# Optimization experiments

Hardware: AMD Instinct MI355X
Metric: run time of the kernel (lower is better)

The kernel has to match this reference:

```python
import jax, jax.numpy as jnp
import numpy as np

B, C, H, W = 8, 128, 192, 192
CROP = 39
LEN = CROP // 2            # 19 -> 38x38 crop
CY = CX = 96               # fixed crop center (original draws random.randint(19, 173))
MARGIN = 1.0


def grid_sample_bilinear(img, grid):
    """Bilinear grid_sample, align_corners=True, zeros padding.
    img: (B,C,H,W); grid: (B,H,W,2) with (x,y) in [-1,1]."""
    _, _, Hi, Wi = img.shape
    gx = (grid[..., 0] + 1.0) * 0.5 * (Wi - 1)   # (B,H,W) source x
    gy = (grid[..., 1] + 1.0) * 0.5 * (Hi - 1)   # (B,H,W) source y
    x0 = jnp.floor(gx)
    y0 = jnp.floor(gy)

    def gather(xf, yf):
        valid = (xf >= 0) & (xf <= Wi - 1) & (yf >= 0) & (yf <= Hi - 1)
        xi = jnp.clip(xf, 0, Wi - 1).astype(jnp.int32)
        yi = jnp.clip(yf, 0, Hi - 1).astype(jnp.int32)
        # per-batch gather: (C,H,W) values at integer (y,x) locations
        v = jax.vmap(lambda im, y, x: im[:, y, x])(img, yi, xi)  # (B,C,H,W)
        return v * valid[:, None, :, :].astype(img.dtype)

    wx1 = gx - x0
    wx0 = 1.0 - wx1
    wy1 = gy - y0
    wy0 = 1.0 - wy1
    w = lambda a: a[:, None, :, :]
    return (w(wx0 * wy0) * gather(x0,       y0)
          + w(wx1 * wy0) * gather(x0 + 1.0, y0)
          + w(wx0 * wy1) * gather(x0,       y0 + 1.0)
          + w(wx1 * wy1) * gather(x0 + 1.0, y0 + 1.0))


def hardnet_loss(anchor, positive, margin=MARGIN):
    """loss_HardNet with anchor_swap=False, batch_reduce='min', triplet_margin."""
    d1 = jnp.sum(anchor * anchor, axis=1)                       # (N,)
    d2 = jnp.sum(positive * positive, axis=1)                   # (N,)
    sq = d1[:, None] + d2[None, :] - 2.0 * (anchor @ positive.T)  # (N,N)
    dm = jnp.sqrt(jnp.maximum(sq, 0.0) + 1e-6) + 1e-8
    n = dm.shape[0]
    pos = jnp.diagonal(dm)                                      # positive distances
    dmod = dm + jnp.eye(n, dtype=dm.dtype) * 10.0               # mask diagonal
    dmod = dmod + jnp.where(dmod < 0.008, 10.0, 0.0)            # mask near-duplicates
    min_neg = jnp.min(dmod, axis=1)                             # hardest negative per anchor
    return jnp.mean(jnp.maximum(margin + pos - min_neg, 0.0))


def setup_inputs() -> dict:
    key = jax.random.key(0)
    k1, k2, k3 = jax.random.split(key, 3)
    feat1 = jax.random.normal(k1, (B, C, H, W), dtype=jnp.float32)
    feat2 = jax.random.normal(k2, (B, C, H, W), dtype=jnp.float32)
    # absolute flow: pixel coordinates in [0, W-1] / [0, H-1]
    aflow = jax.random.uniform(k3, (B, 2, H, W), dtype=jnp.float32) * (W - 1)
    return {"feat1": feat1, "feat2": feat2, "aflow": aflow}


def reference(feat1, feat2, aflow):
    # _aflow_to_grid: pixel coords -> [-1,1] grid (align_corners=True convention)
    gx = aflow[:, 0] * (2.0 / (W - 1)) - 1.0
    gy = aflow[:, 1] * (2.0 / (H - 1)) - 1.0
    grid = jnp.stack([gx, gy], axis=-1)                          # (B,H,W,2)
    grid = jnp.where(jnp.isnan(grid), 9e9, grid)                 # invalid -> out of range
    feat2to1 = grid_sample_bilinear(feat2, grid)                 # warp img2 feats to img1
    s = slice(CY - LEN, CY + LEN)                                # fixed 38x38 crop
    f1 = feat1[:, :, s, s]
    f2 = feat2to1[:, :, s, s]
    a = f1.transpose(0, 2, 3, 1).reshape(-1, C)                  # (B*38*38, C)
    p = f2.transpose(0, 2, 3, 1).reshape(-1, C)
    return hardnet_loss(a, p)
```

## Files before the change

### kernel.cpp

```cpp
#include <hip/hip_runtime.h>
#include <stdint.h>

#define Hh 192
#define Ww 192
#define HW 36864
#define CROPW 38
#define CW2 1444
#define CROPOFF 77
#define NPTS 11552
#define NPAD 11776
#define NTT 46
#define NCT 92
#define NG 5
#define JPB 19
#define NBLK (NG*NTT)
#define CROPB 304
#define CRDB 46
#define BIGF 3.0e38f

typedef short bf16x8 __attribute__((ext_vector_type(8)));
typedef float f32x4 __attribute__((ext_vector_type(4)));
typedef uint32_t u32x2 __attribute__((ext_vector_type(2)));
typedef uint32_t u32x4 __attribute__((ext_vector_type(4)));
typedef unsigned short ushort;

__device__ __forceinline__ ushort f2bf(float f) {
  uint32_t b = __float_as_uint(f);
  uint32_t r = b + 0x7fffu + ((b >> 16) & 1u);
  return (ushort)(r >> 16);
}
__device__ __forceinline__ float bf2f(ushort u) {
  return __uint_as_float(((uint32_t)u) << 16);
}

__device__ __forceinline__ void g2l16(const void* g, void* l) {
  __builtin_amdgcn_global_load_lds(
      (const __attribute__((address_space(1))) unsigned int*)g,
      (__attribute__((address_space(3))) unsigned int*)l, 16, 0, 0);
}

__global__ __launch_bounds__(256) void prep2_k(
    const float* __restrict__ feat1, const float* __restrict__ aflow,
    ushort* __restrict__ aB, u32x4* __restrict__ coords) {
  int bid = blockIdx.x;
  int t = threadIdx.x;
  if (bid < CROPB) {
    __shared__ __align__(16) ushort lsh[38*136];
    int b = bid / CROPW, r = bid % CROPW;
    int y = CROPOFF + r;
    {
      int xo = t & 63, c0 = t >> 6;
      if (xo < CROPW) {
        const float* src = feat1 + ((size_t)b*128*HW) + (size_t)y*Ww + CROPOFF + xo;
        #pragma unroll
        for (int k = 0; k < 32; ++k) {
          int cc = c0*32 + k;
          lsh[xo*136 + cc] = f2bf(src[(size_t)cc*HW]);
        }
      }
    }
    __syncthreads();
    int chunk = t & 7, p0 = t >> 3;
    #pragma unroll
    for (int pp = 0; pp < 2; ++pp) {
      int p = p0 + pp*32;
      if (p >= CROPW) break;
      int idx = b*CW2 + r*CROPW + p;
      ushort* dst = aB + (size_t)idx*128 + chunk*16;
      *(bf16x8*)dst       = *(const bf16x8*)&lsh[p*136 + chunk*16];
      *(bf16x8*)(dst + 8) = *(const bf16x8*)&lsh[p*136 + chunk*16 + 8];
    }
  } else {
    int idx = (bid - CROPB)*256 + t;
    if (idx >= NPTS) return;
    int b = idx / CW2;
    int rem = idx % CW2;
    int r = rem / CROPW, cx = rem % CROPW;
    int y = CROPOFF + r, x = CROPOFF + cx;
    float ax = aflow[((b*2 + 0)*Hh + y)*Ww + x];
    float ay = aflow[((b*2 + 1)*Hh + y)*Ww + x];
    float gxn = ax * (2.0f/(Ww-1)) - 1.0f;
    float gyn = ay * (2.0f/(Hh-1)) - 1.0f;
    float gx = (gxn + 1.0f) * 0.5f * (Ww-1);
    float gy = (gyn + 1.0f) * 0.5f * (Hh-1);
    int xi = min((int)floorf(gx), Ww-2);
    int yi = min((int)floorf(gy), Hh-2);
    u32x4 cd;
    cd.x = (uint32_t)(yi*Ww + xi);
    cd.y = __float_as_uint(gx - (float)xi);
    cd.z = __float_as_uint(gy - (float)yi);
    cd.w = 0;
    coords[idx] = cd;
  }
}

__global__ __launch_bounds__(256) void slab_k(
    const float* __restrict__ feat2, const u32x4* __restrict__ coords,
    ushort* __restrict__ pB) {
  __shared__ __align__(16) ushort plane[HW];
  int bid = blockIdx.x;
  int b = bid >> 7, c = bid & 127;
  int t = threadIdx.x;
  const float* src = feat2 + ((size_t)(b*128 + c)) * HW;
  #pragma unroll
  for (int k = 0; k < 36; ++k) {
    int i = (k*256 + t) * 4;
    f32x4 v = *(const f32x4*)(src + i);
    u32x2 pk;
    pk.x = (uint32_t)f2bf(v[0]) | ((uint32_t)f2bf(v[1]) << 16);
    pk.y = (uint32_t)f2bf(v[2]) | ((uint32_t)f2bf(v[3]) << 16);
    *(u32x2*)&plane[i] = pk;
  }
  __syncthreads();
  int pbase = b*CW2;
  #pragma unroll
  for (int it = 0; it < 6; ++it) {
    int p = it*256 + t;
    if (p < CW2) {
      u32x4 cd = coords[pbase + p];
      int cell = (int)cd.x;
      float wx1 = __uint_as_float(cd.y), wx0 = 1.f - wx1;
      float wy1 = __uint_as_float(cd.z), wy0 = 1.f - wy1;
      float v00 = bf2f(plane[cell]);
      float v01 = bf2f(plane[cell + 1]);
      float v10 = bf2f(plane[cell + Ww]);
      float v11 = bf2f(plane[cell + Ww + 1]);
      float v = wy0*(wx0*v00 + wx1*v01) + wy1*(wx0*v10 + wx1*v11);
      pB[(size_t)(pbase + p)*128 + c] = f2bf(v);
    }
  }
}

__global__ __launch_bounds__(256) void d12_k(
    ushort* __restrict__ aB, ushort* __restrict__ pB,
    float* __restrict__ d1, float* __restrict__ d2) {
  int w = threadIdx.x >> 6, l = threadIdx.x & 63;
  int base = blockIdx.x*32 + w*8;
  #pragma unroll
  for (int i = 0; i < 8; ++i) {
    int row = base + i;
    if (row < NPTS) {
      uint32_t ua = *(const uint32_t*)&aB[(size_t)row*128 + l*2];
      uint32_t up = *(const uint32_t*)&pB[(size_t)row*128 + l*2];
      float a0 = bf2f((ushort)ua), a1 = bf2f((ushort)(ua >> 16));
      float p0 = bf2f((ushort)up), p1 = bf2f((ushort)(up >> 16));
      float sa = a0*a0 + a1*a1;
      float sp = p0*p0 + p1*p1;
      for (int off = 1; off < 64; off <<= 1) {
        sa += __shfl_xor(sa, off);
        sp += __shfl_xor(sp, off);
      }
      if (l == 0) { d1[row] = sa; d2[row] = sp; }
    } else {
      *(uint32_t*)&aB[(size_t)row*128 + l*2] = 0;
      *(uint32_t*)&pB[(size_t)row*128 + l*2] = 0;
      if (l == 0) { d1[row] = 0.f; d2[row] = 1e30f; }
    }
  }
}

__global__ __launch_bounds__(512) void gemmp_k(
    const ushort* __restrict__ aB, const ushort* __restrict__ pB,
    const float* __restrict__ d1, const float* __restrict__ d2,
    float* __restrict__ pos, float* __restrict__ pmin) {
  __shared__ __align__(16) ushort lB[2][128*128];

  int bid = blockIdx.x;
  int xcd = bid & 7, kk = bid >> 3;
  int start = (xcd < 6) ? xcd*29 : 174 + (xcd-6)*28;
  int L = start + kk;
  int g = L / NTT, tM = L % NTT;
  int j0 = g * JPB;
  int jn = (NCT - j0 < JPB) ? (NCT - j0) : JPB;

  int tid = threadIdx.x;
  int rowg = tid >> 4, cb = (tid & 15) << 4;
  int w = tid >> 6, l = tid & 63;
  int wr = w >> 1, wc = w & 1;
  int lcol = l & 15, hq = l >> 4, rb = hq << 2;
  int rsw = (lcol & 7) << 4;

  {
    const char* gB = (const char*)pB + (size_t)j0 * 128 * 256;
    #pragma unroll
    for (int rnd = 0; rnd < 4; ++rnd) {
      int row = rnd*32 + rowg;
      g2l16(gB + row*256 + (cb ^ ((row&7)<<4)), (char*)lB[0] + row*256 + cb);
    }
  }

  bf16x8 aF[16];
  {
    const char* gA = (const char*)aB + ((size_t)(tM*256 + wr*64 + lcol))*256 + hq*16;
    #pragma unroll
    for (int ma = 0; ma < 4; ++ma)
      #pragma unroll
      for (int ks = 0; ks < 4; ++ks)
        aF[ma*4+ks] = *(const bf16x8*)(gA + ma*16*256 + ks*64);
  }
  __syncthreads();

  float mPart[4] = {BIGF, BIGF, BIGF, BIGF};

  for (int it = 0; it < jn; ++it) {
    int j = j0 + it;
    if (it + 1 < jn) {
      const char* gB = (const char*)pB + (size_t)(j+1) * 128 * 256;
      char* dst = (char*)lB[(it+1) & 1];
      #pragma unroll
      for (int rnd = 0; rnd < 4; ++rnd) {
        int row = rnd*32 + rowg;
        g2l16(gB + row*256 + (cb ^ ((row&7)<<4)), dst + row*256 + cb);
      }
    }
    const char* bufB = (const char*)lB[it & 1];
    f32x4 acc[4][4] = {};
    #pragma unroll
    for (int ks = 0; ks < 4; ++ks) {
      int cbase = ks*64 + (hq << 4);
      bf16x8 bF[4];
      #pragma unroll
      for (int np = 0; np < 4; ++np)
        bF[np] = *(const bf16x8*)(bufB + (wc*64 + np*16 + lcol)*256 + (cbase ^ rsw));
      #pragma unroll
      for (int np = 0; np < 4; ++np)
        #pragma unroll
        for (int ma = 0; ma < 4; ++ma)
          acc[np][ma] = __builtin_amdgcn_mfma_f32_16x16x32_bf16(bF[np], aF[ma*4+ks], acc[np][ma], 0, 0, 0);
    }

    f32x4 d2v[4];
    #pragma unroll
    for (int np = 0; np < 4; ++np)
      d2v[np] = *(const f32x4*)&d2[j*128 + wc*64 + np*16 + rb];

    if ((j >> 1) != tM) {
      #pragma unroll
      for (int ma = 0; ma < 4; ++ma)
        #pragma unroll
        for (int np = 0; np < 4; ++np)
          #pragma unroll
          for (int reg = 0; reg < 4; ++reg)
            mPart[ma] = fminf(mPart[ma], fmaf(-2.f, acc[np][ma][reg], d2v[np][reg]));
    } else {
      #pragma unroll
      for (int ma = 0; ma < 4; ++ma) {
        int gi = tM*256 + wr*64 + ma*16 + lcol;
        #pragma unroll
        for (int np = 0; np < 4; ++np)
          #pragma unroll
          for (int reg = 0; reg < 4; ++reg) {
            int gj = j*128 + wc*64 + np*16 + rb + reg;
            float t = fmaf(-2.f, acc[np][ma][reg], d2v[np][reg]);
            if (gi == gj)
              pos[gi] = sqrtf(fmaxf(d1[gi] + t, 0.f) + 1e-6f) + 1e-8f;
            else
              mPart[ma] = fminf(mPart[ma], t);
          }
      }
    }
    __syncthreads();
  }

  #pragma unroll
  for (int ma = 0; ma < 4; ++ma) {
    float u = mPart[ma];
    u = fminf(u, __shfl_xor(u, 16));
    u = fminf(u, __shfl_xor(u, 32));
    mPart[ma] = u;
  }
  __syncthreads();
  float* sm = (float*)lB;
  if (hq == 0) {
    #pragma unroll
    for (int ma = 0; ma < 4; ++ma)
      sm[wc*256 + wr*64 + ma*16 + lcol] = mPart[ma];
  }
  __syncthreads();
  if (tid < 256) {
    int row = tM*256 + tid;
    float u = fminf(sm[tid], sm[256 + tid]);
    pmin[g*NPAD + row] = sqrtf(fmaxf(d1[row] + u, 0.f) + 1e-6f) + 1e-8f;
  }
}

__global__ __launch_bounds__(1024) void fin_k(const float* __restrict__ pos,
                                              const float* __restrict__ pmin,
                                              float* __restrict__ out) {
  float s = 0.f;
  for (int i = threadIdx.x; i < NPTS; i += 1024) {
    float p = pos[i];
    float mneg = p + 10.f;
    #pragma unroll
    for (int g = 0; g < NG; ++g) mneg = fminf(mneg, pmin[g*NPAD + i]);
    s += fmaxf(1.0f + p - mneg, 0.f);
  }
  for (int off = 1; off < 64; off <<= 1) s += __shfl_xor(s, off);
  __shared__ float red[16];
  if ((threadIdx.x & 63) == 0) red[threadIdx.x >> 6] = s;
  __syncthreads();
  if (threadIdx.x == 0) {
    float t = 0.f;
    #pragma unroll
    for (int k = 0; k < 16; ++k) t += red[k];
    out[0] = t / (float)NPTS;
  }
}

extern "C" void kernel_launch(void* const* d_in, const int* in_sizes, int n_in,
                              void* d_out, int out_size, void* d_ws, size_t ws_size,
                              hipStream_t stream) {
  const float* feat1 = (const float*)d_in[0];
  const float* feat2 = (const float*)d_in[1];
  const float* aflow = (const float*)d_in[2];

  char* ws = (char*)d_ws;
  ushort* aB = (ushort*)ws;
  ushort* pB = aB + (size_t)NPAD * 128;
  float*  d1 = (float*)(pB + (size_t)NPAD * 128);
  float*  d2 = d1 + NPAD;
  float*  pos = d2 + NPAD;
  float*  pmin = pos + NPAD;
  u32x4*  coords = (u32x4*)(pmin + (size_t)NG*NPAD);

  hipLaunchKernelGGL(prep2_k, dim3(CROPB + CRDB), dim3(256), 0, stream,
                     feat1, aflow, aB, coords);
  hipLaunchKernelGGL(slab_k, dim3(1024), dim3(256), 0, stream,
                     feat2, coords, pB);
  hipLaunchKernelGGL(d12_k, dim3(NPAD/32), dim3(256), 0, stream,
                     aB, pB, d1, d2);
  hipLaunchKernelGGL(gemmp_k, dim3(NBLK), dim3(512), 0, stream,
                     aB, pB, d1, d2, pos, pmin);
  hipLaunchKernelGGL(fin_k, dim3(1), dim3(1024), 0, stream,
                     pos, pmin, (float*)d_out);
}
```

Before: 98.19 us.

## Fuse norm computation into prep and warp kernels, pair channels, shrink GEMM tiles

```diff
diff --git a/kernel.cpp b/kernel.cpp
--- a/kernel.cpp
+++ b/kernel.cpp
@@ -9,11 +9,11 @@
 #define CROPOFF 77
 #define NPTS 11552
 #define NPAD 11776
-#define NTT 46
+#define NMT 92
 #define NCT 92
 #define NG 5
 #define JPB 19
-#define NBLK (NG*NTT)
+#define NBLK (NG*NMT)
 #define CROPB 304
 #define CRDB 46
 #define BIGF 3.0e38f
@@ -41,7 +41,9 @@
 
 __global__ __launch_bounds__(256) void prep2_k(
     const float* __restrict__ feat1, const float* __restrict__ aflow,
-    ushort* __restrict__ aB, u32x4* __restrict__ coords) {
+    ushort* __restrict__ aB, ushort* __restrict__ pB,
+    float* __restrict__ d1, float* __restrict__ d2,
+    u32x4* __restrict__ coords) {
   int bid = blockIdx.x;
   int t = threadIdx.x;
   if (bid < CROPB) {
@@ -69,10 +71,19 @@
       ushort* dst = aB + (size_t)idx*128 + chunk*16;
       *(bf16x8*)dst       = *(const bf16x8*)&lsh[p*136 + chunk*16];
       *(bf16x8*)(dst + 8) = *(const bf16x8*)&lsh[p*136 + chunk*16 + 8];
-    }
-  } else {
+      float s = 0.f;
+      #pragma unroll
+      for (int j = 0; j < 16; ++j) {
+        float v = bf2f(lsh[p*136 + chunk*16 + j]);
+        s += v*v;
+      }
+      s += __shfl_xor(s, 1); s += __shfl_xor(s, 2); s += __shfl_xor(s, 4);
+      if (chunk == 0) d1[idx] = s;
+    }
+  } else if (bid < CROPB + CRDB) {
     int idx = (bid - CROPB)*256 + t;
     if (idx >= NPTS) return;
+    d2[idx] = 0.f;
     int b = idx / CW2;
     int rem = idx % CW2;
     int r = rem / CROPW, cx = rem % CROPW;
@@ -91,25 +102,42 @@
     cd.z = __float_as_uint(gy - (float)yi);
     cd.w = 0;
     coords[idx] = cd;
+  } else {
+    if (t < NPAD - NPTS) {
+      int row = NPTS + t;
+      u32x4 z = {0,0,0,0};
+      #pragma unroll
+      for (int c = 0; c < 8; ++c) {
+        *(u32x4*)&aB[(size_t)row*128 + c*16] = z;
+        *(u32x4*)&aB[(size_t)row*128 + c*16 + 8] = z;
+        *(u32x4*)&pB[(size_t)row*128 + c*16] = z;
+        *(u32x4*)&pB[(size_t)row*128 + c*16 + 8] = z;
+      }
+      d1[row] = 0.f;
+      d2[row] = 1e30f;
+    }
   }
 }
 
 __global__ __launch_bounds__(256) void slab_k(
     const float* __restrict__ feat2, const u32x4* __restrict__ coords,
-    ushort* __restrict__ pB) {
-  __shared__ __align__(16) ushort plane[HW];
+    ushort* __restrict__ pB, float* __restrict__ d2) {
+  __shared__ __align__(16) uint32_t plane[HW];
   int bid = blockIdx.x;
-  int b = bid >> 7, c = bid & 127;
+  int b = bid >> 6, cp = bid & 63, c = cp*2;
   int t = threadIdx.x;
-  const float* src = feat2 + ((size_t)(b*128 + c)) * HW;
-  #pragma unroll
+  const float* srcA = feat2 + ((size_t)(b*128 + c)) * HW;
+  const float* srcB = srcA + HW;
+  #pragma unroll 6
   for (int k = 0; k < 36; ++k) {
     int i = (k*256 + t) * 4;
-    f32x4 v = *(const f32x4*)(src + i);
-    u32x2 pk;
-    pk.x = (uint32_t)f2bf(v[0]) | ((uint32_t)f2bf(v[1]) << 16);
-    pk.y = (uint32_t)f2bf(v[2]) | ((uint32_t)f2bf(v[3]) << 16);
-    *(u32x2*)&plane[i] = pk;
+    f32x4 va = *(const f32x4*)(srcA + i);
+    f32x4 vb = *(const f32x4*)(srcB + i);
+    u32x4 pk;
+    #pragma unroll
+    for (int j = 0; j < 4; ++j)
+      pk[j] = (uint32_t)f2bf(va[j]) | ((uint32_t)f2bf(vb[j]) << 16);
+    *(u32x4*)&plane[i] = pk;
   }
   __syncthreads();
   int pbase = b*CW2;
@@ -121,45 +149,23 @@
       int cell = (int)cd.x;
       float wx1 = __uint_as_float(cd.y), wx0 = 1.f - wx1;
       float wy1 = __uint_as_float(cd.z), wy0 = 1.f - wy1;
-      float v00 = bf2f(plane[cell]);
-      float v01 = bf2f(plane[cell + 1]);
-      float v10 = bf2f(plane[cell + Ww]);
-      float v11 = bf2f(plane[cell + Ww + 1]);
-      float v = wy0*(wx0*v00 + wx1*v01) + wy1*(wx0*v10 + wx1*v11);
-      pB[(size_t)(pbase + p)*128 + c] = f2bf(v);
-    }
-  }
-}
-
-__global__ __launch_bounds__(256) void d12_k(
-    ushort* __restrict__ aB, ushort* __restrict__ pB,
-    float* __restrict__ d1, float* __restrict__ d2) {
-  int w = threadIdx.x >> 6, l = threadIdx.x & 63;
-  int base = blockIdx.x*32 + w*8;
-  #pragma unroll
-  for (int i = 0; i < 8; ++i) {
-    int row = base + i;
-    if (row < NPTS) {
-      uint32_t ua = *(const uint32_t*)&aB[(size_t)row*128 + l*2];
-      uint32_t up = *(const uint32_t*)&pB[(size_t)row*128 + l*2];
-      float a0 = bf2f((ushort)ua), a1 = bf2f((ushort)(ua >> 16));
-      float p0 = bf2f((ushort)up), p1 = bf2f((ushort)(up >> 16));
-      float sa = a0*a0 + a1*a1;
-      float sp = p0*p0 + p1*p1;
-      for (int off = 1; off < 64; off <<= 1) {
-        sa += __shfl_xor(sa, off);
-        sp += __shfl_xor(sp, off);
-      }
-      if (l == 0) { d1[row] = sa; d2[row] = sp; }
-    } else {
-      *(uint32_t*)&aB[(size_t)row*128 + l*2] = 0;
-      *(uint32_t*)&pB[(size_t)row*128 + l*2] = 0;
-      if (l == 0) { d1[row] = 0.f; d2[row] = 1e30f; }
-    }
-  }
-}
-
-__global__ __launch_bounds__(512) void gemmp_k(
+      uint32_t u00 = plane[cell];
+      uint32_t u01 = plane[cell + 1];
+      uint32_t u10 = plane[cell + Ww];
+      uint32_t u11 = plane[cell + Ww + 1];
+      float v0 = wy0*(wx0*bf2f((ushort)u00) + wx1*bf2f((ushort)u01))
+               + wy1*(wx0*bf2f((ushort)u10) + wx1*bf2f((ushort)u11));
+      float v1 = wy0*(wx0*bf2f((ushort)(u00>>16)) + wx1*bf2f((ushort)(u01>>16)))
+               + wy1*(wx0*bf2f((ushort)(u10>>16)) + wx1*bf2f((ushort)(u11>>16)));
+      ushort q0 = f2bf(v0), q1 = f2bf(v1);
+      *(uint32_t*)&pB[(size_t)(pbase + p)*128 + c] = (uint32_t)q0 | ((uint32_t)q1 << 16);
+      float f0 = bf2f(q0), f1 = bf2f(q1);
+      atomicAdd(&d2[pbase + p], f0*f0 + f1*f1);
+    }
+  }
+}
+
+__global__ __launch_bounds__(256) void gemmp_k(
     const ushort* __restrict__ aB, const ushort* __restrict__ pB,
     const float* __restrict__ d1, const float* __restrict__ d2,
     float* __restrict__ pos, float* __restrict__ pmin) {
@@ -167,9 +173,9 @@
 
   int bid = blockIdx.x;
   int xcd = bid & 7, kk = bid >> 3;
-  int start = (xcd < 6) ? xcd*29 : 174 + (xcd-6)*28;
+  int start = (xcd < 4) ? xcd*58 : 232 + (xcd-4)*57;
   int L = start + kk;
-  int g = L / NTT, tM = L % NTT;
+  int g = L / NMT, tM = L % NMT;
   int j0 = g * JPB;
   int jn = (NCT - j0 < JPB) ? (NCT - j0) : JPB;
 
@@ -183,15 +189,15 @@
   {
     const char* gB = (const char*)pB + (size_t)j0 * 128 * 256;
     #pragma unroll
-    for (int rnd = 0; rnd < 4; ++rnd) {
-      int row = rnd*32 + rowg;
+    for (int rnd = 0; rnd < 8; ++rnd) {
+      int row = rnd*16 + rowg;
       g2l16(gB + row*256 + (cb ^ ((row&7)<<4)), (char*)lB[0] + row*256 + cb);
     }
   }
 
   bf16x8 aF[16];
   {
-    const char* gA = (const char*)aB + ((size_t)(tM*256 + wr*64 + lcol))*256 + hq*16;
+    const char* gA = (const char*)aB + ((size_t)(tM*128 + wr*64 + lcol))*256 + hq*16;
     #pragma unroll
     for (int ma = 0; ma < 4; ++ma)
       #pragma unroll
@@ -208,11 +214,16 @@
       const char* gB = (const char*)pB + (size_t)(j+1) * 128 * 256;
       char* dst = (char*)lB[(it+1) & 1];
       #pragma unroll
-      for (int rnd = 0; rnd < 4; ++rnd) {
-        int row = rnd*32 + rowg;
+      for (int rnd = 0; rnd < 8; ++rnd) {
+        int row = rnd*16 + rowg;
         g2l16(gB + row*256 + (cb ^ ((row&7)<<4)), dst + row*256 + cb);
       }
     }
+    f32x4 d2v[4];
+    #pragma unroll
+    for (int np = 0; np < 4; ++np)
+      d2v[np] = *(const f32x4*)&d2[j*128 + wc*64 + np*16 + rb];
+
     const char* bufB = (const char*)lB[it & 1];
     f32x4 acc[4][4] = {};
     #pragma unroll
@@ -229,12 +240,7 @@
           acc[np][ma] = __builtin_amdgcn_mfma_f32_16x16x32_bf16(bF[np], aF[ma*4+ks], acc[np][ma], 0, 0, 0);
     }
 
-    f32x4 d2v[4];
-    #pragma unroll
-    for (int np = 0; np < 4; ++np)
-      d2v[np] = *(const f32x4*)&d2[j*128 + wc*64 + np*16 + rb];
-
-    if ((j >> 1) != tM) {
+    if (j != tM) {
       #pragma unroll
       for (int ma = 0; ma < 4; ++ma)
         #pragma unroll
@@ -245,7 +251,7 @@
     } else {
       #pragma unroll
       for (int ma = 0; ma < 4; ++ma) {
-        int gi = tM*256 + wr*64 + ma*16 + lcol;
+        int gi = tM*128 + wr*64 + ma*16 + lcol;
         #pragma unroll
         for (int np = 0; np < 4; ++np)
           #pragma unroll
@@ -274,12 +280,12 @@
   if (hq == 0) {
     #pragma unroll
     for (int ma = 0; ma < 4; ++ma)
-      sm[wc*256 + wr*64 + ma*16 + lcol] = mPart[ma];
-  }
-  __syncthreads();
-  if (tid < 256) {
-    int row = tM*256 + tid;
-    float u = fminf(sm[tid], sm[256 + tid]);
+      sm[wc*128 + wr*64 + ma*16 + lcol] = mPart[ma];
+  }
+  __syncthreads();
+  if (tid < 128) {
+    int row = tM*128 + tid;
+    float u = fminf(sm[tid], sm[128 + tid]);
     pmin[g*NPAD + row] = sqrtf(fmaxf(d1[row] + u, 0.f) + 1e-6f) + 1e-8f;
   }
 }
@@ -323,13 +329,11 @@
   float*  pmin = pos + NPAD;
   u32x4*  coords = (u32x4*)(pmin + (size_t)NG*NPAD);
 
-  hipLaunchKernelGGL(prep2_k, dim3(CROPB + CRDB), dim3(256), 0, stream,
-                     feat1, aflow, aB, coords);
-  hipLaunchKernelGGL(slab_k, dim3(1024), dim3(256), 0, stream,
-                     feat2, coords, pB);
-  hipLaunchKernelGGL(d12_k, dim3(NPAD/32), dim3(256), 0, stream,
-                     aB, pB, d1, d2);
-  hipLaunchKernelGGL(gemmp_k, dim3(NBLK), dim3(512), 0, stream,
+  hipLaunchKernelGGL(prep2_k, dim3(CROPB + CRDB + 1), dim3(256), 0, stream,
+                     feat1, aflow, aB, pB, d1, d2, coords);
+  hipLaunchKernelGGL(slab_k, dim3(512), dim3(256), 0, stream,
+                     feat2, coords, pB, d2);
+  hipLaunchKernelGGL(gemmp_k, dim3(NBLK), dim3(256), 0, stream,
                      aB, pB, d1, d2, pos, pmin);
   hipLaunchKernelGGL(fin_k, dim3(1), dim3(1024), 0, stream,
                      pos, pmin, (float*)d_out);
```

Result: faster. 93.72 us (-4.6%).
